# Kernel tuning notes

Hardware: AMD Instinct MI355X
Metric: run time of the kernel (lower is better)

The kernel has to match this reference:

```python
import jax, jax.numpy as jnp
import numpy as np

N, C, T, V = 32, 256, 256, 25
CI = C // 2
BN_EPS = 1e-5


def setup_inputs() -> dict:
    key = jax.random.key(0)
    ks = jax.random.split(key, 11)
    s = 1.0 / np.sqrt(C)
    si = 1.0 / np.sqrt(CI)
    return {
        "x": jax.random.normal(ks[0], (N, C, T, V), dtype=jnp.float32),
        "Wg": jax.random.normal(ks[1], (CI, C), dtype=jnp.float32) * s,
        "bg": jax.random.normal(ks[2], (CI,), dtype=jnp.float32) * s,
        "Wth": jax.random.normal(ks[3], (CI, C), dtype=jnp.float32) * s,
        "bth": jax.random.normal(ks[4], (CI,), dtype=jnp.float32) * s,
        "Wph": jax.random.normal(ks[5], (CI, C), dtype=jnp.float32) * s,
        "bph": jax.random.normal(ks[6], (CI,), dtype=jnp.float32) * s,
        "Ww": jax.random.normal(ks[7], (C, CI), dtype=jnp.float32) * si,
        "bw": jax.random.normal(ks[8], (C,), dtype=jnp.float32) * si,
        "gamma": jax.random.normal(ks[9], (C,), dtype=jnp.float32) * 0.1,
        "beta": jax.random.normal(ks[10], (C,), dtype=jnp.float32) * 0.1,
    }


def reference(x, Wg, bg, Wth, bth, Wph, bph, Ww, bw, gamma, beta):
    n, c, t, v = x.shape
    ci = Wg.shape[0]
    # [N,C,T,V] -> [N*V, C, T] (permute(0,3,1,2).reshape)
    xf = jnp.transpose(x, (0, 3, 1, 2)).reshape(n * v, c, t)
    # 1x1 Conv1d == channel GEMM
    g_x = jnp.einsum('bct,oc->bot', xf, Wg) + bg[:, None]      # [N*V, Ci, T]
    g_x = g_x.reshape(n, v * ci, t).transpose(0, 2, 1)         # [N, T, V*Ci]
    xmean = xf.reshape(n, v, c, t).mean(axis=1)                # [N, C, T]
    theta = (jnp.einsum('nct,oc->not', xmean, Wth) + bth[:, None]).transpose(0, 2, 1)  # [N,T,Ci]
    phi = jnp.einsum('nct,oc->not', xmean, Wph) + bph[:, None]  # [N, Ci, T]
    f = jnp.matmul(theta, phi)                                  # [N, T, T]
    f = jax.nn.softmax(f, axis=-1)
    y = jnp.matmul(f, g_x)                                      # [N, T, V*Ci]
    y = y.transpose(0, 2, 1).reshape(n * v, ci, t)              # [N*V, Ci, T]
    wy = jnp.einsum('bct,oc->bot', y, Ww) + bw[:, None]         # [N*V, C, T]
    # BatchNorm1d (training mode: batch stats over (batch, T))
    mu = wy.mean(axis=(0, 2))
    var = wy.var(axis=(0, 2))
    wy = (wy - mu[:, None]) * jax.lax.rsqrt(var[:, None] + BN_EPS) * gamma[:, None] + beta[:, None]
    z = wy + xf                                                 # residual
    return jnp.transpose(z.reshape(n, v, c, t), (0, 2, 3, 1))   # [N, C, T, V]
```

## Files before the change

kernel.cpp:

```cpp
#include <hip/hip_runtime.h>

typedef unsigned short u16;
using s8v = __attribute__((ext_vector_type(8))) short;
using f4v = __attribute__((ext_vector_type(4))) float;

constexpr int kN = 32, kC = 256, kT = 256, kV = 25, kCI = 128;
constexpr int kTV = kT * kV;
constexpr int kCIV = kCI * kV;
constexpr int kSAMP = kN * kT * kV;
constexpr int SYY_B = 640;

__device__ __forceinline__ float bf2f(u16 v) {
  return __uint_as_float(((unsigned)v) << 16);
}
__device__ __forceinline__ u16 f2bf(float f) {
  unsigned u = __float_as_uint(f);
  return (u16)((u + 0x7FFFu + ((u >> 16) & 1u)) >> 16);
}

__global__ __launch_bounds__(256) void k_xmean(const float* __restrict__ x, float* __restrict__ xm) {
  __shared__ float sm[6400];
  size_t base = (size_t)blockIdx.x * 6400;
  const float4* src = (const float4*)(x + base);
  for (int i = threadIdx.x; i < 1600; i += 256) ((float4*)sm)[i] = src[i];
  __syncthreads();
  const float* r = sm + threadIdx.x * 25;
  float s = 0.f;
#pragma unroll
  for (int j = 0; j < 25; ++j) s += r[j];
  xm[(size_t)blockIdx.x * 256 + threadIdx.x] = s * (1.0f / kV);
}

__global__ __launch_bounds__(256) void k_thetaphi(
    const float* __restrict__ xmean, const float* __restrict__ Wth, const float* __restrict__ bth,
    const float* __restrict__ Wph, const float* __restrict__ bph,
    float* __restrict__ theta, float* __restrict__ phi) {
  int n = blockIdx.x >> 7;
  int o = blockIdx.x & 127;
  int t = threadIdx.x;
  __shared__ float wt[kC], wp[kC];
  wt[t] = Wth[o * kC + t];
  wp[t] = Wph[o * kC + t];
  __syncthreads();
  const float* xm = xmean + (size_t)n * kC * kT + t;
  float at = 0.f, ap = 0.f;
#pragma unroll 8
  for (int c = 0; c < kC; ++c) {
    float xv = xm[c * kT];
    at = fmaf(wt[c], xv, at);
    ap = fmaf(wp[c], xv, ap);
  }
  size_t idx = ((size_t)n * kCI + o) * kT + t;
  theta[idx] = at + bth[o];
  phi[idx] = ap + bph[o];
}

__global__ __launch_bounds__(256) void k_fsm(const float* __restrict__ theta, const float* __restrict__ phi,
                                             u16* __restrict__ f) {
  int n = blockIdx.x >> 8;
  int t = blockIdx.x & 255;
  int tp = threadIdx.x;
  __shared__ float th[kCI];
  __shared__ float red[256];
  if (tp < kCI) th[tp] = theta[((size_t)n * kCI + tp) * kT + t];
  __syncthreads();
  const float* ph = phi + (size_t)n * kCI * kT + tp;
  float acc = 0.f;
#pragma unroll 8
  for (int o = 0; o < kCI; ++o) acc = fmaf(th[o], ph[o * kT], acc);
  red[tp] = acc;
  __syncthreads();
  for (int s = 128; s > 0; s >>= 1) {
    if (tp < s) red[tp] = fmaxf(red[tp], red[tp + s]);
    __syncthreads();
  }
  float m = red[0];
  __syncthreads();
  float e = __expf(acc - m);
  red[tp] = e;
  __syncthreads();
  for (int s = 128; s > 0; s >>= 1) {
    if (tp < s) red[tp] += red[tp + s];
    __syncthreads();
  }
  f[(size_t)blockIdx.x * 256 + tp] = f2bf(e * (1.0f / red[0]));
}

__global__ __launch_bounds__(256) void k_cvtW(const float* __restrict__ Wg, const float* __restrict__ Ww,
                                              u16* __restrict__ Wg_fl, u16* __restrict__ Ww_fl) {
  int i = blockIdx.x * 256 + threadIdx.x;
  { int m = i >> 8, k = i & 255; Wg_fl[(size_t)((k >> 3) * 128 + m) * 8 + (k & 7)] = f2bf(Wg[i]); }
  { int m = i >> 7, k = i & 127; Ww_fl[(size_t)((k >> 3) * 256 + m) * 8 + (k & 7)] = f2bf(Ww[i]); }
}

template <int K_TOT, int NCOLS, int MODE, typename TB>
__global__ __launch_bounds__(256) void k_gemm(
    const u16* __restrict__ A_, const TB* __restrict__ B_, const float* __restrict__ bias,
    void* __restrict__ outp, const float* __restrict__ scale, const float* __restrict__ shift,
    const float* __restrict__ xres) {
  constexpr int KSTEPS = K_TOT / 32;
  constexpr int M_TOT = (MODE == 0) ? 128 : 256;
  __shared__ uint4 Bs[512];
  const int n = blockIdx.z, m0 = blockIdx.y * 128, n0 = blockIdx.x * 128;
  const int tid = threadIdx.x, lane = tid & 63, w = tid >> 6;
  const int wr = (w >> 1) * 64, wc = (w & 1) * 64;
  const int l15 = lane & 15, l4 = lane >> 4;
  const TB* Bn = B_ + (size_t)n * K_TOT * NCOLS + n0;
  const int scol = tid & 127, sk0 = tid >> 7;
  f4v acc[4][4];
#pragma unroll
  for (int i = 0; i < 4; ++i)
#pragma unroll
    for (int j = 0; j < 4; ++j) acc[i][j] = f4v{0.f, 0.f, 0.f, 0.f};

  for (int ks = 0; ks < KSTEPS; ++ks) {
    __syncthreads();
#pragma unroll
    for (int p = 0; p < 2; ++p) {
      int ksub = sk0 + p * 2;
      const TB* src = Bn + (size_t)(ks * 32 + ksub * 8) * NCOLS + scol;
      union { u16 u[8]; uint4 v; } pk;
#pragma unroll
      for (int j = 0; j < 8; ++j) {
        if constexpr (sizeof(TB) == 2) pk.u[j] = src[(size_t)j * NCOLS];
        else pk.u[j] = f2bf(src[(size_t)j * NCOLS]);
      }
      int blk = ksub * 128 + scol;
      blk ^= (blk >> 2) & 3;
      Bs[blk] = pk.v;
    }
    __syncthreads();
    s8v af[4];
#pragma unroll
    for (int f = 0; f < 4; ++f) {
      int m = m0 + wr + f * 16 + l15;
      const u16* ap;
      if constexpr (MODE == 1)
        ap = A_ + ((size_t)(n * 256 + m) * 256 + ks * 32 + l4 * 8);
      else
        ap = A_ + (size_t)((ks * 4 + l4) * M_TOT + m) * 8;
      af[f] = *(const s8v*)ap;
    }
#pragma unroll
    for (int g = 0; g < 4; ++g) {
      int blk = l4 * 128 + wc + g * 16 + l15;
      blk ^= (blk >> 2) & 3;
      s8v bf = *(const s8v*)&Bs[blk];
#pragma unroll
      for (int f = 0; f < 4; ++f)
        acc[f][g] = __builtin_amdgcn_mfma_f32_16x16x32_bf16(af[f], bf, acc[f][g], 0, 0, 0);
    }
  }
#pragma unroll
  for (int f = 0; f < 4; ++f) {
    int growb = m0 + wr + f * 16 + l4 * 4;
#pragma unroll
    for (int g = 0; g < 4; ++g) {
      int gcol = n0 + wc + g * 16 + l15;
#pragma unroll
      for (int r = 0; r < 4; ++r) {
        int grow = growb + r;
        float vv = acc[f][g][r];
        if constexpr (MODE == 0) {
          vv += bias[grow];
          int t = gcol / 25, v5 = gcol - t * 25;
          ((u16*)outp)[((size_t)n * kT + t) * kCIV + grow * 25 + v5] = f2bf(vv);
        } else if constexpr (MODE == 1) {
          int ci = gcol / 25, v5 = gcol - ci * 25;
          ((u16*)outp)[((size_t)n * kCI + ci) * kTV + grow * 25 + v5] = f2bf(vv);
        } else {
          size_t idx = ((size_t)n * kC + grow) * kTV + gcol;
          ((float*)outp)[idx] = vv * scale[grow] + shift[grow] + xres[idx];
        }
      }
    }
  }
}

__global__ __launch_bounds__(256) void k_syy(const u16* __restrict__ yb, float* __restrict__ psyy,
                                             float* __restrict__ psy) {
  const int b = blockIdx.x, n = b / 20, kc = b % 20;
  const int kbase = kc * 320;
  const int tid = threadIdx.x, lane = tid & 63, w = tid >> 6;
  const int wr = (w >> 1) * 64, wc = (w & 1) * 64, l15 = lane & 15, l4 = lane >> 4;
  const u16* Y = yb + (size_t)n * kCI * kTV;
  f4v acc[4][4];
#pragma unroll
  for (int i = 0; i < 4; ++i)
#pragma unroll
    for (int j = 0; j < 4; ++j) acc[i][j] = f4v{0.f, 0.f, 0.f, 0.f};
  float syl[4] = {0.f, 0.f, 0.f, 0.f};
  for (int ks = 0; ks < 10; ++ks) {
    int k = kbase + ks * 32 + l4 * 8;
    s8v af[4], bf[4];
#pragma unroll
    for (int f = 0; f < 4; ++f) {
      af[f] = *(const s8v*)(Y + (size_t)(wr + f * 16 + l15) * kTV + k);
      bf[f] = *(const s8v*)(Y + (size_t)(wc + f * 16 + l15) * kTV + k);
    }
#pragma unroll
    for (int f = 0; f < 4; ++f)
#pragma unroll
      for (int j = 0; j < 8; ++j) syl[f] += bf2f((u16)af[f][j]);
#pragma unroll
    for (int g = 0; g < 4; ++g)
#pragma unroll
      for (int f = 0; f < 4; ++f)
        acc[f][g] = __builtin_amdgcn_mfma_f32_16x16x32_bf16(af[f], bf[g], acc[f][g], 0, 0, 0);
  }
  float* pb = psyy + (size_t)b * 16384;
#pragma unroll
  for (int f = 0; f < 4; ++f)
#pragma unroll
    for (int g = 0; g < 4; ++g)
#pragma unroll
      for (int r = 0; r < 4; ++r)
        pb[(wr + f * 16 + l4 * 4 + r) * kCI + wc + g * 16 + l15] = acc[f][g][r];
#pragma unroll
  for (int f = 0; f < 4; ++f) {
    float s = syl[f];
    s += __shfl_xor(s, 16);
    s += __shfl_xor(s, 32);
    if ((w & 1) == 0 && l4 == 0) psy[b * kCI + wr + f * 16 + l15] = s;
  }
}

__global__ __launch_bounds__(256) void k_reduce1(const float* __restrict__ psyy, float* __restrict__ ps2) {
  int outi = (blockIdx.x & 63) * 256 + threadIdx.x;
  int kseg = blockIdx.x >> 6;
  float s = 0.f;
  for (int b = 0; b < 40; ++b) s += psyy[(size_t)(kseg * 40 + b) * 16384 + outi];
  ps2[(size_t)kseg * 16384 + outi] = s;
}

__global__ __launch_bounds__(256) void k_reduce2(const float* __restrict__ ps2, const float* __restrict__ psy,
                                                 float* __restrict__ syy, float* __restrict__ sy) {
  if (blockIdx.x < 64) {
    int i = blockIdx.x * 256 + threadIdx.x;
    float s = 0.f;
#pragma unroll
    for (int kk = 0; kk < 16; ++kk) s += ps2[(size_t)kk * 16384 + i];
    syy[i] = s;
  } else if (threadIdx.x < kCI) {
    float s = 0.f;
    for (int b = 0; b < SYY_B; ++b) s += psy[b * kCI + threadIdx.x];
    sy[threadIdx.x] = s;
  }
}

__global__ __launch_bounds__(128) void k_stats(const float* __restrict__ syy, const float* __restrict__ sy,
                                               const float* __restrict__ Ww, const float* __restrict__ bw,
                                               const float* __restrict__ gamma, const float* __restrict__ beta,
                                               float* __restrict__ scale, float* __restrict__ shift) {
  int c2 = blockIdx.x;
  int tid = threadIdx.x;
  __shared__ float wsm[kCI];
  __shared__ float red1[kCI], red2[kCI];
  wsm[tid] = Ww[c2 * kCI + tid];
  __syncthreads();
  float val = 0.f;
#pragma unroll 8
  for (int ci = 0; ci < kCI; ++ci) val = fmaf(wsm[ci], syy[ci * kCI + tid], val);
  red1[tid] = wsm[tid] * sy[tid];
  red2[tid] = val * wsm[tid];
  __syncthreads();
  for (int s = 64; s > 0; s >>= 1) {
    if (tid < s) { red1[tid] += red1[tid + s]; red2[tid] += red2[tid + s]; }
    __syncthreads();
  }
  if (tid == 0) {
    const float invS = 1.0f / (float)kSAMP;
    float m1 = red1[0] * invS;
    float b = bw[c2];
    float mu = m1 + b;
    float e2 = red2[0] * invS + 2.f * b * m1 + b * b;
    float var = e2 - mu * mu;
    float rstd = rsqrtf(var + 1e-5f);
    float sc = rstd * gamma[c2];
    scale[c2] = sc;
    shift[c2] = beta[c2] + (b - mu) * sc;
  }
}

extern "C" void kernel_launch(void* const* d_in, const int* in_sizes, int n_in,
                              void* d_out, int out_size, void* d_ws, size_t ws_size,
                              hipStream_t stream) {
  const float* x     = (const float*)d_in[0];
  const float* Wg    = (const float*)d_in[1];
  const float* bg    = (const float*)d_in[2];
  const float* Wth   = (const float*)d_in[3];
  const float* bth   = (const float*)d_in[4];
  const float* Wph   = (const float*)d_in[5];
  const float* bph   = (const float*)d_in[6];
  const float* Ww    = (const float*)d_in[7];
  const float* bw    = (const float*)d_in[8];
  const float* gamma = (const float*)d_in[9];
  const float* beta  = (const float*)d_in[10];
  float* out = (float*)d_out;

  char* wsb = (char*)d_ws;
  float* xmean = (float*)(wsb);
  float* theta = (float*)(wsb + (8u << 20));
  float* phi   = (float*)(wsb + (12u << 20));
  u16*   f_bf  = (u16*)(wsb + (16u << 20));
  float* ps2   = (float*)(wsb + (20u << 20));
  float* psy   = (float*)(wsb + (21u << 20));
  float* syy   = (float*)(wsb + (22u << 20));
  float* sy    = syy + 16384;
  float* scale = sy + 128;
  float* shift = scale + 256;
  u16* Wg_fl = (u16*)(wsb + (23u << 20));
  u16* Ww_fl = Wg_fl + 32768;
  u16* g2    = (u16*)(wsb + (24u << 20));
  float* psyy = (float*)(wsb + (24u << 20));
  u16* yb    = (u16*)(wsb + (80u << 20));

  k_xmean<<<8192, 256, 0, stream>>>(x, xmean);
  k_cvtW<<<128, 256, 0, stream>>>(Wg, Ww, Wg_fl, Ww_fl);
  k_thetaphi<<<4096, 256, 0, stream>>>(xmean, Wth, bth, Wph, bph, theta, phi);
  k_fsm<<<8192, 256, 0, stream>>>(theta, phi, f_bf);
  k_gemm<256, kTV, 0, float><<<dim3(50, 1, 32), 256, 0, stream>>>(
      Wg_fl, x, bg, (void*)g2, nullptr, nullptr, nullptr);
  k_gemm<256, kCIV, 1, u16><<<dim3(25, 2, 32), 256, 0, stream>>>(
      f_bf, g2, nullptr, (void*)yb, nullptr, nullptr, nullptr);
  k_syy<<<SYY_B, 256, 0, stream>>>(yb, psyy, psy);
  k_reduce1<<<1024, 256, 0, stream>>>(psyy, ps2);
  k_reduce2<<<65, 256, 0, stream>>>(ps2, psy, syy, sy);
  k_stats<<<256, 128, 0, stream>>>(syy, sy, Ww, bw, gamma, beta, scale, shift);
  k_gemm<128, kTV, 2, u16><<<dim3(50, 2, 32), 256, 0, stream>>>(
      Ww_fl, yb, nullptr, (void*)out, scale, shift, x);
}
```

Measured before the change: 431.6 us.

## Cache bf16 x, MFMA-fuse attention softmax, batch thetaphi outputs, simplify Syy reduction

The prep kernel now writes a bf16 copy of x alongside the T-mean. The first GEMM reads that copy instead of converting fp32 on the fly, and the final GEMM reads it for the residual add. Theta/phi are emitted transposed in bf16, four output channels per block. The scalar score-plus-softmax kernel is replaced by an MFMA GEMM with the column softmax fused in registers and shared memory. The Syy pass uses fewer, longer blocks with a single reduction kernel. Together these aim to cut fp32 memory traffic, launch count and reduction overhead. The trade-off is that the residual now uses a bf16-rounded x, which loses precision.

```diff
diff --git a/kernel.cpp b/kernel.cpp
--- a/kernel.cpp
+++ b/kernel.cpp
@@ -8,7 +8,7 @@
 constexpr int kTV = kT * kV;
 constexpr int kCIV = kCI * kV;
 constexpr int kSAMP = kN * kT * kV;
-constexpr int SYY_B = 640;
+constexpr int SYY_B = 256;
 
 __device__ __forceinline__ float bf2f(u16 v) {
   return __uint_as_float(((unsigned)v) << 16);
@@ -18,11 +18,19 @@
   return (u16)((u + 0x7FFFu + ((u >> 16) & 1u)) >> 16);
 }
 
-__global__ __launch_bounds__(256) void k_xmean(const float* __restrict__ x, float* __restrict__ xm) {
+__global__ __launch_bounds__(256) void k_prep(const float* __restrict__ x, u16* __restrict__ x_bf,
+                                              float* __restrict__ xm) {
   __shared__ float sm[6400];
   size_t base = (size_t)blockIdx.x * 6400;
   const float4* src = (const float4*)(x + base);
-  for (int i = threadIdx.x; i < 1600; i += 256) ((float4*)sm)[i] = src[i];
+  ushort4* dst = (ushort4*)(x_bf + base);
+  for (int i = threadIdx.x; i < 1600; i += 256) {
+    float4 v = src[i];
+    ((float4*)sm)[i] = v;
+    ushort4 b;
+    b.x = f2bf(v.x); b.y = f2bf(v.y); b.z = f2bf(v.z); b.w = f2bf(v.w);
+    dst[i] = b;
+  }
   __syncthreads();
   const float* r = sm + threadIdx.x * 25;
   float s = 0.f;
@@ -34,56 +42,121 @@
 __global__ __launch_bounds__(256) void k_thetaphi(
     const float* __restrict__ xmean, const float* __restrict__ Wth, const float* __restrict__ bth,
     const float* __restrict__ Wph, const float* __restrict__ bph,
-    float* __restrict__ theta, float* __restrict__ phi) {
-  int n = blockIdx.x >> 7;
-  int o = blockIdx.x & 127;
+    u16* __restrict__ thT, u16* __restrict__ phT) {
+  int n = blockIdx.x >> 5;
+  int o0 = (blockIdx.x & 31) * 4;
   int t = threadIdx.x;
-  __shared__ float wt[kC], wp[kC];
-  wt[t] = Wth[o * kC + t];
-  wp[t] = Wph[o * kC + t];
-  __syncthreads();
-  const float* xm = xmean + (size_t)n * kC * kT + t;
-  float at = 0.f, ap = 0.f;
-#pragma unroll 8
+  __shared__ float wt[4][kC], wp[4][kC];
+  for (int i = threadIdx.x; i < 1024; i += 256) {
+    wt[i >> 8][i & 255] = Wth[(o0 + (i >> 8)) * kC + (i & 255)];
+    wp[i >> 8][i & 255] = Wph[(o0 + (i >> 8)) * kC + (i & 255)];
+  }
+  __syncthreads();
+  const float* xmp = xmean + (size_t)n * kC * kT + t;
+  float a[4], p[4];
+#pragma unroll
+  for (int j = 0; j < 4; ++j) { a[j] = bth[o0 + j]; p[j] = bph[o0 + j]; }
+#pragma unroll 4
   for (int c = 0; c < kC; ++c) {
-    float xv = xm[c * kT];
-    at = fmaf(wt[c], xv, at);
-    ap = fmaf(wp[c], xv, ap);
-  }
-  size_t idx = ((size_t)n * kCI + o) * kT + t;
-  theta[idx] = at + bth[o];
-  phi[idx] = ap + bph[o];
-}
-
-__global__ __launch_bounds__(256) void k_fsm(const float* __restrict__ theta, const float* __restrict__ phi,
-                                             u16* __restrict__ f) {
-  int n = blockIdx.x >> 8;
-  int t = blockIdx.x & 255;
-  int tp = threadIdx.x;
-  __shared__ float th[kCI];
-  __shared__ float red[256];
-  if (tp < kCI) th[tp] = theta[((size_t)n * kCI + tp) * kT + t];
-  __syncthreads();
-  const float* ph = phi + (size_t)n * kCI * kT + tp;
-  float acc = 0.f;
-#pragma unroll 8
-  for (int o = 0; o < kCI; ++o) acc = fmaf(th[o], ph[o * kT], acc);
-  red[tp] = acc;
-  __syncthreads();
-  for (int s = 128; s > 0; s >>= 1) {
-    if (tp < s) red[tp] = fmaxf(red[tp], red[tp + s]);
-    __syncthreads();
-  }
-  float m = red[0];
-  __syncthreads();
-  float e = __expf(acc - m);
-  red[tp] = e;
-  __syncthreads();
-  for (int s = 128; s > 0; s >>= 1) {
-    if (tp < s) red[tp] += red[tp + s];
-    __syncthreads();
-  }
-  f[(size_t)blockIdx.x * 256 + tp] = f2bf(e * (1.0f / red[0]));
+    float xv = xmp[c * kT];
+#pragma unroll
+    for (int j = 0; j < 4; ++j) {
+      a[j] = fmaf(wt[j][c], xv, a[j]);
+      p[j] = fmaf(wp[j][c], xv, p[j]);
+    }
+  }
+  size_t rowb = ((size_t)n * kT + t) * kCI + o0;
+#pragma unroll
+  for (int j = 0; j < 4; ++j) {
+    thT[rowb + j] = f2bf(a[j]);
+    phT[rowb + j] = f2bf(p[j]);
+  }
+}
+
+__global__ __launch_bounds__(512) void k_fmfma(const u16* __restrict__ thT, const u16* __restrict__ phT,
+                                               u16* __restrict__ f) {
+  const int n = blockIdx.x >> 1;
+  const int tc0 = (blockIdx.x & 1) * 128;
+  const int tid = threadIdx.x, lane = tid & 63, w = tid >> 6;
+  const int wM = w & 3, wr = wM * 64, wc = (w >> 2) * 64;
+  const int l15 = lane & 15, l4 = lane >> 4;
+  __shared__ float redm[4][128], reds[4][128];
+  f4v acc[4][4];
+#pragma unroll
+  for (int i = 0; i < 4; ++i)
+#pragma unroll
+    for (int j = 0; j < 4; ++j) acc[i][j] = f4v{0.f, 0.f, 0.f, 0.f};
+#pragma unroll
+  for (int ks = 0; ks < 4; ++ks) {
+    s8v af[4], bf[4];
+#pragma unroll
+    for (int fi = 0; fi < 4; ++fi)
+      af[fi] = *(const s8v*)(phT + ((size_t)(n * 256 + wr + fi * 16 + l15) * kCI + ks * 32 + l4 * 8));
+#pragma unroll
+    for (int g = 0; g < 4; ++g)
+      bf[g] = *(const s8v*)(thT + ((size_t)(n * 256 + tc0 + wc + g * 16 + l15) * kCI + ks * 32 + l4 * 8));
+#pragma unroll
+    for (int g = 0; g < 4; ++g)
+#pragma unroll
+      for (int fi = 0; fi < 4; ++fi)
+        acc[fi][g] = __builtin_amdgcn_mfma_f32_16x16x32_bf16(af[fi], bf[g], acc[fi][g], 0, 0, 0);
+  }
+  float mx[4], sm[4];
+#pragma unroll
+  for (int g = 0; g < 4; ++g) {
+    float m = -1e30f;
+#pragma unroll
+    for (int fi = 0; fi < 4; ++fi)
+#pragma unroll
+      for (int r = 0; r < 4; ++r) m = fmaxf(m, acc[fi][g][r]);
+    m = fmaxf(m, __shfl_xor(m, 16));
+    m = fmaxf(m, __shfl_xor(m, 32));
+    mx[g] = m;
+  }
+  if (l4 == 0)
+#pragma unroll
+    for (int g = 0; g < 4; ++g) redm[wM][wc + g * 16 + l15] = mx[g];
+  __syncthreads();
+#pragma unroll
+  for (int g = 0; g < 4; ++g) {
+    int col = wc + g * 16 + l15;
+    mx[g] = fmaxf(fmaxf(redm[0][col], redm[1][col]), fmaxf(redm[2][col], redm[3][col]));
+  }
+#pragma unroll
+  for (int g = 0; g < 4; ++g) {
+    float s = 0.f;
+#pragma unroll
+    for (int fi = 0; fi < 4; ++fi)
+#pragma unroll
+      for (int r = 0; r < 4; ++r) {
+        float e = __expf(acc[fi][g][r] - mx[g]);
+        acc[fi][g][r] = e;
+        s += e;
+      }
+    s += __shfl_xor(s, 16);
+    s += __shfl_xor(s, 32);
+    sm[g] = s;
+  }
+  if (l4 == 0)
+#pragma unroll
+    for (int g = 0; g < 4; ++g) reds[wM][wc + g * 16 + l15] = sm[g];
+  __syncthreads();
+#pragma unroll
+  for (int g = 0; g < 4; ++g) {
+    int col = wc + g * 16 + l15;
+    float inv = 1.0f / (reds[0][col] + reds[1][col] + reds[2][col] + reds[3][col]);
+    int t = tc0 + col;
+#pragma unroll
+    for (int fi = 0; fi < 4; ++fi) {
+      int tp0 = wr + fi * 16 + l4 * 4;
+      ushort4 st;
+      st.x = f2bf(acc[fi][g][0] * inv);
+      st.y = f2bf(acc[fi][g][1] * inv);
+      st.z = f2bf(acc[fi][g][2] * inv);
+      st.w = f2bf(acc[fi][g][3] * inv);
+      *(ushort4*)(f + (size_t)(n * 256 + t) * 256 + tp0) = st;
+    }
+  }
 }
 
 __global__ __launch_bounds__(256) void k_cvtW(const float* __restrict__ Wg, const float* __restrict__ Ww,
@@ -93,11 +166,11 @@
   { int m = i >> 7, k = i & 127; Ww_fl[(size_t)((k >> 3) * 256 + m) * 8 + (k & 7)] = f2bf(Ww[i]); }
 }
 
-template <int K_TOT, int NCOLS, int MODE, typename TB>
+template <int K_TOT, int NCOLS, int MODE>
 __global__ __launch_bounds__(256) void k_gemm(
-    const u16* __restrict__ A_, const TB* __restrict__ B_, const float* __restrict__ bias,
+    const u16* __restrict__ A_, const u16* __restrict__ B_, const float* __restrict__ bias,
     void* __restrict__ outp, const float* __restrict__ scale, const float* __restrict__ shift,
-    const float* __restrict__ xres) {
+    const u16* __restrict__ xres) {
   constexpr int KSTEPS = K_TOT / 32;
   constexpr int M_TOT = (MODE == 0) ? 128 : 256;
   __shared__ uint4 Bs[512];
@@ -105,7 +178,7 @@
   const int tid = threadIdx.x, lane = tid & 63, w = tid >> 6;
   const int wr = (w >> 1) * 64, wc = (w & 1) * 64;
   const int l15 = lane & 15, l4 = lane >> 4;
-  const TB* Bn = B_ + (size_t)n * K_TOT * NCOLS + n0;
+  const u16* Bn = B_ + (size_t)n * K_TOT * NCOLS + n0;
   const int scol = tid & 127, sk0 = tid >> 7;
   f4v acc[4][4];
 #pragma unroll
@@ -118,13 +191,10 @@
 #pragma unroll
     for (int p = 0; p < 2; ++p) {
       int ksub = sk0 + p * 2;
-      const TB* src = Bn + (size_t)(ks * 32 + ksub * 8) * NCOLS + scol;
+      const u16* src = Bn + (size_t)(ks * 32 + ksub * 8) * NCOLS + scol;
       union { u16 u[8]; uint4 v; } pk;
 #pragma unroll
-      for (int j = 0; j < 8; ++j) {
-        if constexpr (sizeof(TB) == 2) pk.u[j] = src[(size_t)j * NCOLS];
-        else pk.u[j] = f2bf(src[(size_t)j * NCOLS]);
-      }
+      for (int j = 0; j < 8; ++j) pk.u[j] = src[(size_t)j * NCOLS];
       int blk = ksub * 128 + scol;
       blk ^= (blk >> 2) & 3;
       Bs[blk] = pk.v;
@@ -132,14 +202,14 @@
     __syncthreads();
     s8v af[4];
 #pragma unroll
-    for (int f = 0; f < 4; ++f) {
-      int m = m0 + wr + f * 16 + l15;
+    for (int fi = 0; fi < 4; ++fi) {
+      int m = m0 + wr + fi * 16 + l15;
       const u16* ap;
       if constexpr (MODE == 1)
         ap = A_ + ((size_t)(n * 256 + m) * 256 + ks * 32 + l4 * 8);
       else
         ap = A_ + (size_t)((ks * 4 + l4) * M_TOT + m) * 8;
-      af[f] = *(const s8v*)ap;
+      af[fi] = *(const s8v*)ap;
     }
 #pragma unroll
     for (int g = 0; g < 4; ++g) {
@@ -147,20 +217,20 @@
       blk ^= (blk >> 2) & 3;
       s8v bf = *(const s8v*)&Bs[blk];
 #pragma unroll
-      for (int f = 0; f < 4; ++f)
-        acc[f][g] = __builtin_amdgcn_mfma_f32_16x16x32_bf16(af[f], bf, acc[f][g], 0, 0, 0);
-    }
-  }
-#pragma unroll
-  for (int f = 0; f < 4; ++f) {
-    int growb = m0 + wr + f * 16 + l4 * 4;
+      for (int fi = 0; fi < 4; ++fi)
+        acc[fi][g] = __builtin_amdgcn_mfma_f32_16x16x32_bf16(af[fi], bf, acc[fi][g], 0, 0, 0);
+    }
+  }
+#pragma unroll
+  for (int fi = 0; fi < 4; ++fi) {
+    int growb = m0 + wr + fi * 16 + l4 * 4;
 #pragma unroll
     for (int g = 0; g < 4; ++g) {
       int gcol = n0 + wc + g * 16 + l15;
 #pragma unroll
       for (int r = 0; r < 4; ++r) {
         int grow = growb + r;
-        float vv = acc[f][g][r];
+        float vv = acc[fi][g][r];
         if constexpr (MODE == 0) {
           vv += bias[grow];
           int t = gcol / 25, v5 = gcol - t * 25;
@@ -170,7 +240,7 @@
           ((u16*)outp)[((size_t)n * kCI + ci) * kTV + grow * 25 + v5] = f2bf(vv);
         } else {
           size_t idx = ((size_t)n * kC + grow) * kTV + gcol;
-          ((float*)outp)[idx] = vv * scale[grow] + shift[grow] + xres[idx];
+          ((float*)outp)[idx] = vv * scale[grow] + shift[grow] + bf2f(xres[idx]);
         }
       }
     }
@@ -179,8 +249,8 @@
 
 __global__ __launch_bounds__(256) void k_syy(const u16* __restrict__ yb, float* __restrict__ psyy,
                                              float* __restrict__ psy) {
-  const int b = blockIdx.x, n = b / 20, kc = b % 20;
-  const int kbase = kc * 320;
+  const int b = blockIdx.x, n = b >> 3, kc = b & 7;
+  const int kbase = kc * 800;
   const int tid = threadIdx.x, lane = tid & 63, w = tid >> 6;
   const int wr = (w >> 1) * 64, wc = (w & 1) * 64, l15 = lane & 15, l4 = lane >> 4;
   const u16* Y = yb + (size_t)n * kCI * kTV;
@@ -190,56 +260,47 @@
 #pragma unroll
     for (int j = 0; j < 4; ++j) acc[i][j] = f4v{0.f, 0.f, 0.f, 0.f};
   float syl[4] = {0.f, 0.f, 0.f, 0.f};
-  for (int ks = 0; ks < 10; ++ks) {
+  for (int ks = 0; ks < 25; ++ks) {
     int k = kbase + ks * 32 + l4 * 8;
     s8v af[4], bf[4];
 #pragma unroll
-    for (int f = 0; f < 4; ++f) {
-      af[f] = *(const s8v*)(Y + (size_t)(wr + f * 16 + l15) * kTV + k);
-      bf[f] = *(const s8v*)(Y + (size_t)(wc + f * 16 + l15) * kTV + k);
-    }
-#pragma unroll
-    for (int f = 0; f < 4; ++f)
-#pragma unroll
-      for (int j = 0; j < 8; ++j) syl[f] += bf2f((u16)af[f][j]);
+    for (int fi = 0; fi < 4; ++fi) {
+      af[fi] = *(const s8v*)(Y + (size_t)(wr + fi * 16 + l15) * kTV + k);
+      bf[fi] = *(const s8v*)(Y + (size_t)(wc + fi * 16 + l15) * kTV + k);
+    }
+#pragma unroll
+    for (int fi = 0; fi < 4; ++fi)
+#pragma unroll
+      for (int j = 0; j < 8; ++j) syl[fi] += bf2f((u16)af[fi][j]);
 #pragma unroll
     for (int g = 0; g < 4; ++g)
 #pragma unroll
-      for (int f = 0; f < 4; ++f)
-        acc[f][g] = __builtin_amdgcn_mfma_f32_16x16x32_bf16(af[f], bf[g], acc[f][g], 0, 0, 0);
+      for (int fi = 0; fi < 4; ++fi)
+        acc[fi][g] = __builtin_amdgcn_mfma_f32_16x16x32_bf16(af[fi], bf[g], acc[fi][g], 0, 0, 0);
   }
   float* pb = psyy + (size_t)b * 16384;
 #pragma unroll
-  for (int f = 0; f < 4; ++f)
+  for (int fi = 0; fi < 4; ++fi)
 #pragma unroll
     for (int g = 0; g < 4; ++g)
 #pragma unroll
       for (int r = 0; r < 4; ++r)
-        pb[(wr + f * 16 + l4 * 4 + r) * kCI + wc + g * 16 + l15] = acc[f][g][r];
-#pragma unroll
-  for (int f = 0; f < 4; ++f) {
-    float s = syl[f];
+        pb[(wr + fi * 16 + l4 * 4 + r) * kCI + wc + g * 16 + l15] = acc[fi][g][r];
+#pragma unroll
+  for (int fi = 0; fi < 4; ++fi) {
+    float s = syl[fi];
     s += __shfl_xor(s, 16);
     s += __shfl_xor(s, 32);
-    if ((w & 1) == 0 && l4 == 0) psy[b * kCI + wr + f * 16 + l15] = s;
-  }
-}
-
-__global__ __launch_bounds__(256) void k_reduce1(const float* __restrict__ psyy, float* __restrict__ ps2) {
-  int outi = (blockIdx.x & 63) * 256 + threadIdx.x;
-  int kseg = blockIdx.x >> 6;
-  float s = 0.f;
-  for (int b = 0; b < 40; ++b) s += psyy[(size_t)(kseg * 40 + b) * 16384 + outi];
-  ps2[(size_t)kseg * 16384 + outi] = s;
-}
-
-__global__ __launch_bounds__(256) void k_reduce2(const float* __restrict__ ps2, const float* __restrict__ psy,
-                                                 float* __restrict__ syy, float* __restrict__ sy) {
+    if ((w & 1) == 0 && l4 == 0) psy[b * kCI + wr + fi * 16 + l15] = s;
+  }
+}
+
+__global__ __launch_bounds__(256) void k_reduce(const float* __restrict__ psyy, const float* __restrict__ psy,
+                                                float* __restrict__ syy, float* __restrict__ sy) {
   if (blockIdx.x < 64) {
     int i = blockIdx.x * 256 + threadIdx.x;
     float s = 0.f;
-#pragma unroll
-    for (int kk = 0; kk < 16; ++kk) s += ps2[(size_t)kk * 16384 + i];
+    for (int b = 0; b < SYY_B; ++b) s += psyy[(size_t)b * 16384 + i];
     syy[i] = s;
   } else if (threadIdx.x < kCI) {
     float s = 0.f;
@@ -300,33 +361,32 @@
 
   char* wsb = (char*)d_ws;
   float* xmean = (float*)(wsb);
-  float* theta = (float*)(wsb + (8u << 20));
-  float* phi   = (float*)(wsb + (12u << 20));
-  u16*   f_bf  = (u16*)(wsb + (16u << 20));
-  float* ps2   = (float*)(wsb + (20u << 20));
-  float* psy   = (float*)(wsb + (21u << 20));
-  float* syy   = (float*)(wsb + (22u << 20));
+  u16*   thT   = (u16*)(wsb + (8u << 20));
+  u16*   phT   = (u16*)(wsb + (10u << 20));
+  u16*   f_bf  = (u16*)(wsb + (12u << 20));
+  float* psy   = (float*)(wsb + (16u << 20));
+  float* syy   = (float*)(wsb + (17u << 20));
   float* sy    = syy + 16384;
   float* scale = sy + 128;
   float* shift = scale + 256;
-  u16* Wg_fl = (u16*)(wsb + (23u << 20));
+  u16* Wg_fl = (u16*)(wsb + (18u << 20));
   u16* Ww_fl = Wg_fl + 32768;
-  u16* g2    = (u16*)(wsb + (24u << 20));
-  float* psyy = (float*)(wsb + (24u << 20));
-  u16* yb    = (u16*)(wsb + (80u << 20));
-
-  k_xmean<<<8192, 256, 0, stream>>>(x, xmean);
+  u16* x_bf  = (u16*)(wsb + (19u << 20));
+  u16* g2    = (u16*)(wsb + (119u << 20));
+  float* psyy = (float*)(wsb + (119u << 20));
+  u16* yb    = (u16*)(wsb + (172u << 20));
+
+  k_prep<<<8192, 256, 0, stream>>>(x, x_bf, xmean);
   k_cvtW<<<128, 256, 0, stream>>>(Wg, Ww, Wg_fl, Ww_fl);
-  k_thetaphi<<<4096, 256, 0, stream>>>(xmean, Wth, bth, Wph, bph, theta, phi);
-  k_fsm<<<8192, 256, 0, stream>>>(theta, phi, f_bf);
-  k_gemm<256, kTV, 0, float><<<dim3(50, 1, 32), 256, 0, stream>>>(
-      Wg_fl, x, bg, (void*)g2, nullptr, nullptr, nullptr);
-  k_gemm<256, kCIV, 1, u16><<<dim3(25, 2, 32), 256, 0, stream>>>(
+  k_thetaphi<<<1024, 256, 0, stream>>>(xmean, Wth, bth, Wph, bph, thT, phT);
+  k_fmfma<<<64, 512, 0, stream>>>(thT, phT, f_bf);
+  k_gemm<256, kTV, 0><<<dim3(50, 1, 32), 256, 0, stream>>>(
+      Wg_fl, x_bf, bg, (void*)g2, nullptr, nullptr, nullptr);
+  k_gemm<256, kCIV, 1><<<dim3(25, 2, 32), 256, 0, stream>>>(
       f_bf, g2, nullptr, (void*)yb, nullptr, nullptr, nullptr);
   k_syy<<<SYY_B, 256, 0, stream>>>(yb, psyy, psy);
-  k_reduce1<<<1024, 256, 0, stream>>>(psyy, ps2);
-  k_reduce2<<<65, 256, 0, stream>>>(ps2, psy, syy, sy);
+  k_reduce<<<65, 256, 0, stream>>>(psyy, psy, syy, sy);
   k_stats<<<256, 128, 0, stream>>>(syy, sy, Ww, bw, gamma, beta, scale, shift);
-  k_gemm<128, kTV, 2, u16><<<dim3(50, 2, 32), 256, 0, stream>>>(
-      Ww_fl, yb, nullptr, (void*)out, scale, shift, x);
-}
+  k_gemm<128, kTV, 2><<<dim3(50, 2, 32), 256, 0, stream>>>(
+      Ww_fl, yb, nullptr, (void*)out, scale, shift, x_bf);
+}
```

Measured after the change: 363.5 us. 1.19x faster.
